# Kernel tuning notes

Measured on AMD Instinct MI355X. Metric: run time of the kernel, lower is better.

Reference implementation:

```python
import jax, jax.numpy as jnp
import numpy as np

N_NODES = 50000
N_EDGES = 800000
D_IN = 128
D_OUT = 128


def setup_inputs() -> dict:
    key = jax.random.key(0)
    k1, k2, k3, k4, k5 = jax.random.split(key, 5)
    # xavier-uniform-like scale for the two linear layers (gain for relu ~ sqrt(2))
    bound = float(np.sqrt(2.0) * np.sqrt(6.0 / (D_IN + D_OUT)))
    return {
        "feat": jax.random.normal(k1, (N_NODES, D_IN), dtype=jnp.float32),
        "w_neigh": jax.random.uniform(k2, (D_OUT, D_IN), minval=-bound, maxval=bound, dtype=jnp.float32),
        "w_self": jax.random.uniform(k3, (D_OUT, D_IN), minval=-bound, maxval=bound, dtype=jnp.float32),
        "b_self": jnp.zeros((D_OUT,), dtype=jnp.float32),
        "rows": jax.random.randint(k4, (N_EDGES,), 0, N_NODES, dtype=jnp.int32),  # src node per edge
        "cols": jax.random.randint(k5, (N_EDGES,), 0, N_NODES, dtype=jnp.int32),  # dst node per edge
    }


def reference(feat, w_neigh, w_self, b_self, rows, cols):
    n = feat.shape[0]
    # srcdata = fc_neigh(feat): [N, D_OUT]
    srcdata = feat @ w_neigh.T
    # deg[j] = A.sum(0)[j] = in-degree of destination j (column sums)
    deg = jax.ops.segment_sum(jnp.ones_like(cols, dtype=feat.dtype), cols, num_segments=n)
    # dstdata = (A @ diag(deg)^-1).T @ srcdata  ==  mean over incoming src neighbors
    agg = jax.ops.segment_sum(srcdata[rows], cols, num_segments=n)  # [N, D_OUT]
    dstdata = agg / jnp.where(deg > 0, deg, 1.0)[:, None]
    # rst = fc_self(h_self) + dstdata
    return feat @ w_self.T + b_self + dstdata
```

## Files before the change

kernel.cpp:

```cpp
#include <hip/hip_runtime.h>
#include <hip/hip_bf16.h>

#define D 128
#define CAP 64
#define TILE 64

typedef __attribute__((ext_vector_type(8))) short bf16x8;
typedef __attribute__((ext_vector_type(4))) float floatx4;

__device__ __forceinline__ unsigned short f2bf(float f) {
    unsigned int u = __float_as_uint(f);
    return (unsigned short)((u + 0x7fffu + ((u >> 16) & 1u)) >> 16);
}

__global__ __launch_bounds__(256) void zero_kernel(int* __restrict__ p, int n) {
    int i = blockIdx.x * 256 + threadIdx.x;
    if (i < n) p[i] = 0;
}

__global__ __launch_bounds__(256) void prep_fill_kernel(
    const float* __restrict__ feat,
    const float* __restrict__ w_self,
    const float* __restrict__ w_neigh,
    const int* __restrict__ rows,
    const int* __restrict__ cols,
    unsigned short* __restrict__ feat_h,
    unsigned short* __restrict__ ws_h,
    unsigned short* __restrict__ wn_h,
    int* __restrict__ cursor,
    unsigned short* __restrict__ slots,
    int n_nodes, int n_edges)
{
    const int b = blockIdx.x;
    const int tid = threadIdx.x;
    const int role = b % 3;

    if (role < 2) {
        int pb = (b / 3) * 2 + role;
        int i  = pb * 256 + tid;
        if (i < n_nodes * 32) {
            float4 v = *(const float4*)&feat[(long long)4 * i];
            ushort4 o;
            o.x = f2bf(v.x); o.y = f2bf(v.y); o.z = f2bf(v.z); o.w = f2bf(v.w);
            *(ushort4*)&feat_h[(long long)4 * i] = o;
        }
    } else {
        int fb = b / 3;
        int e  = fb * 256 + tid;
        if (e < n_edges) {
            int c = cols[e];
            int p = atomicAdd(&cursor[c], 1);
            if (p < CAP) slots[c * CAP + p] = (unsigned short)rows[e];
        }
        if (fb < 32) {
            int i = fb * 256 + tid;
            int j = i & 4095;
            const float* src = (i < 4096) ? w_self : w_neigh;
            unsigned short* dst = (i < 4096) ? ws_h : wn_h;
            float4 v = *(const float4*)&src[4 * j];
            ushort4 o;
            o.x = f2bf(v.x); o.y = f2bf(v.y); o.z = f2bf(v.z); o.w = f2bf(v.w);
            *(ushort4*)&dst[4 * j] = o;
        }
    }
}

__global__ __launch_bounds__(256, 4) void agg_gemm_kernel(
    const unsigned short* __restrict__ feat_h,
    const int* __restrict__ cursor,
    const unsigned short* __restrict__ slots,
    const unsigned short* __restrict__ ws_h,
    const unsigned short* __restrict__ wn_h,
    const float* __restrict__ b_self,
    float* __restrict__ out,
    int n_nodes)
{
    __shared__ unsigned short s_agg[TILE][136];

    const int tid  = threadIdx.x;
    const int row0 = blockIdx.x * TILE;

    {
        const int ln   = tid & 3;
        const int nl   = tid >> 2;
        const int node = row0 + nl;

        float acc[32];
        #pragma unroll
        for (int i = 0; i < 32; ++i) acc[i] = 0.f;

        int deg = 0;
        if (node < n_nodes) {
            deg = cursor[node];
            if (deg > CAP) deg = CAP;
            const unsigned short* slot = slots + (long long)node * CAP;
            for (int k = 0; k < deg; ++k) {
                int r = slot[k];
                const unsigned short* base = feat_h + (long long)r * D + ln * 32;
                uint4 v0 = *(const uint4*)(base + 0);
                uint4 v1 = *(const uint4*)(base + 8);
                uint4 v2 = *(const uint4*)(base + 16);
                uint4 v3 = *(const uint4*)(base + 24);
                const uint4 vv[4] = {v0, v1, v2, v3};
                #pragma unroll
                for (int c = 0; c < 4; ++c) {
                    acc[c * 8 + 0] += __uint_as_float(vv[c].x << 16);
                    acc[c * 8 + 1] += __uint_as_float(vv[c].x & 0xffff0000u);
                    acc[c * 8 + 2] += __uint_as_float(vv[c].y << 16);
                    acc[c * 8 + 3] += __uint_as_float(vv[c].y & 0xffff0000u);
                    acc[c * 8 + 4] += __uint_as_float(vv[c].z << 16);
                    acc[c * 8 + 5] += __uint_as_float(vv[c].z & 0xffff0000u);
                    acc[c * 8 + 6] += __uint_as_float(vv[c].w << 16);
                    acc[c * 8 + 7] += __uint_as_float(vv[c].w & 0xffff0000u);
                }
            }
            float inv = (deg > 0) ? 1.0f / (float)deg : 0.0f;
            #pragma unroll
            for (int c = 0; c < 4; ++c) {
                ushort4 o0, o1;
                o0.x = f2bf(acc[c * 8 + 0] * inv); o0.y = f2bf(acc[c * 8 + 1] * inv);
                o0.z = f2bf(acc[c * 8 + 2] * inv); o0.w = f2bf(acc[c * 8 + 3] * inv);
                o1.x = f2bf(acc[c * 8 + 4] * inv); o1.y = f2bf(acc[c * 8 + 5] * inv);
                o1.z = f2bf(acc[c * 8 + 6] * inv); o1.w = f2bf(acc[c * 8 + 7] * inv);
                *(ushort4*)&s_agg[nl][ln * 32 + c * 8]     = o0;
                *(ushort4*)&s_agg[nl][ln * 32 + c * 8 + 4] = o1;
            }
        } else {
            #pragma unroll
            for (int c = 0; c < 4; ++c) {
                *(ushort4*)&s_agg[nl][ln * 32 + c * 8]     = (ushort4){0,0,0,0};
                *(ushort4*)&s_agg[nl][ln * 32 + c * 8 + 4] = (ushort4){0,0,0,0};
            }
        }
    }
    __syncthreads();

    const int wave  = tid >> 6;
    const int lane  = tid & 63;
    const int m     = lane & 15;
    const int quad  = lane >> 4;
    const int kq    = quad * 8;
    const int rbase = row0 + wave * 16;

    floatx4 gacc[8];
    #pragma unroll
    for (int nt = 0; nt < 8; ++nt) gacc[nt] = (floatx4){0.f, 0.f, 0.f, 0.f};

    int rA = rbase + m;
    if (rA > n_nodes - 1) rA = n_nodes - 1;

    #pragma unroll
    for (int kt = 0; kt < 4; ++kt) {
        const int k = kt * 32 + kq;
        bf16x8 a = *(const bf16x8*)&feat_h[(long long)rA * D + k];
        #pragma unroll
        for (int nt = 0; nt < 8; ++nt) {
            bf16x8 b = *(const bf16x8*)&ws_h[(nt * 16 + m) * D + k];
            gacc[nt] = __builtin_amdgcn_mfma_f32_16x16x32_bf16(a, b, gacc[nt], 0, 0, 0);
        }
    }
    #pragma unroll
    for (int kt = 0; kt < 4; ++kt) {
        const int k = kt * 32 + kq;
        bf16x8 a = *(const bf16x8*)&s_agg[wave * 16 + m][k];
        #pragma unroll
        for (int nt = 0; nt < 8; ++nt) {
            bf16x8 b = *(const bf16x8*)&wn_h[(nt * 16 + m) * D + k];
            gacc[nt] = __builtin_amdgcn_mfma_f32_16x16x32_bf16(a, b, gacc[nt], 0, 0, 0);
        }
    }

    #pragma unroll
    for (int nt = 0; nt < 8; ++nt) {
        int col = nt * 16 + m;
        float bias = b_self[col];
        #pragma unroll
        for (int r = 0; r < 4; ++r) {
            int row = rbase + quad * 4 + r;
            if (row < n_nodes)
                out[(long long)row * D + col] = gacc[nt][r] + bias;
        }
    }
}

extern "C" void kernel_launch(void* const* d_in, const int* in_sizes, int n_in,
                              void* d_out, int out_size, void* d_ws, size_t ws_size,
                              hipStream_t stream) {
    const float* feat    = (const float*)d_in[0];
    const float* w_neigh = (const float*)d_in[1];
    const float* w_self  = (const float*)d_in[2];
    const float* b_self  = (const float*)d_in[3];
    const int*   rows    = (const int*)d_in[4];
    const int*   cols    = (const int*)d_in[5];
    float* out = (float*)d_out;

    const int n_nodes = in_sizes[0] / D;
    const int n_edges = in_sizes[4];

    unsigned short* feat_h = (unsigned short*)d_ws;
    unsigned short* slots  = feat_h + (size_t)n_nodes * D;
    int* cursor = (int*)(slots + (size_t)n_nodes * CAP);
    unsigned short* ws_h = (unsigned short*)(cursor + n_nodes);
    unsigned short* wn_h = ws_h + 16384;

    zero_kernel<<<(n_nodes + 255) / 256, 256, 0, stream>>>(cursor, n_nodes);

    int nblocks = (n_nodes * 32 + 255) / 256 + (n_edges + 255) / 256;
    prep_fill_kernel<<<nblocks, 256, 0, stream>>>(
        feat, w_self, w_neigh, rows, cols,
        feat_h, ws_h, wn_h, cursor, slots, n_nodes, n_edges);

    agg_gemm_kernel<<<(n_nodes + TILE - 1) / TILE, 256, 0, stream>>>(
        feat_h, cursor, slots, ws_h, wn_h, b_self, out, n_nodes);
}
```

Baseline: 193.4 us.

## Batch neighbor gathers with 8 lanes per node and halve row tile

The aggregation phase now gives each node 8 threads instead of 4, each owning 16 feature columns. Each thread loads 8 neighbor indices at once as a vector and issues up to 8 independent row gathers before accumulating, so more memory requests are in flight. The row tile drops from 64 to 32 nodes, giving more blocks, and the MFMA epilogue splits the 128 output columns across wave pairs. The cost is more blocks each doing less GEMM work and larger per-thread register buffers for the batched loads.

Measured after the change: 192.7 us. Within noise of the previous version (-0.4%).

```diff
diff --git a/kernel.cpp b/kernel.cpp
--- a/kernel.cpp
+++ b/kernel.cpp
@@ -3,7 +3,7 @@
 
 #define D 128
 #define CAP 64
-#define TILE 64
+#define TILE 32
 
 typedef __attribute__((ext_vector_type(8))) short bf16x8;
 typedef __attribute__((ext_vector_type(4))) float floatx4;
@@ -12,6 +12,8 @@
     unsigned int u = __float_as_uint(f);
     return (unsigned short)((u + 0x7fffu + ((u >> 16) & 1u)) >> 16);
 }
+__device__ __forceinline__ float bf_lo(unsigned int u) { return __uint_as_float(u << 16); }
+__device__ __forceinline__ float bf_hi(unsigned int u) { return __uint_as_float(u & 0xffff0000u); }
 
 __global__ __launch_bounds__(256) void zero_kernel(int* __restrict__ p, int n) {
     int i = blockIdx.x * 256 + threadIdx.x;
@@ -81,56 +83,66 @@
     const int row0 = blockIdx.x * TILE;
 
     {
-        const int ln   = tid & 3;
-        const int nl   = tid >> 2;
+        const int ln   = tid & 7;
+        const int nl   = tid >> 3;
         const int node = row0 + nl;
 
-        float acc[32];
-        #pragma unroll
-        for (int i = 0; i < 32; ++i) acc[i] = 0.f;
-
-        int deg = 0;
+        float acc[16];
+        #pragma unroll
+        for (int i = 0; i < 16; ++i) acc[i] = 0.f;
+
         if (node < n_nodes) {
-            deg = cursor[node];
+            int deg = cursor[node];
             if (deg > CAP) deg = CAP;
-            const unsigned short* slot = slots + (long long)node * CAP;
-            for (int k = 0; k < deg; ++k) {
-                int r = slot[k];
-                const unsigned short* base = feat_h + (long long)r * D + ln * 32;
-                uint4 v0 = *(const uint4*)(base + 0);
-                uint4 v1 = *(const uint4*)(base + 8);
-                uint4 v2 = *(const uint4*)(base + 16);
-                uint4 v3 = *(const uint4*)(base + 24);
-                const uint4 vv[4] = {v0, v1, v2, v3};
+            const unsigned short* slotp = slots + (long long)node * CAP;
+
+            for (int k0 = 0; k0 < deg; k0 += 8) {
+                uint4 sc = *(const uint4*)(slotp + k0);
+                unsigned int sv[4] = {sc.x, sc.y, sc.z, sc.w};
+                int cnt = deg - k0; if (cnt > 8) cnt = 8;
+
+                uint4 g[8][2];
                 #pragma unroll
-                for (int c = 0; c < 4; ++c) {
-                    acc[c * 8 + 0] += __uint_as_float(vv[c].x << 16);
-                    acc[c * 8 + 1] += __uint_as_float(vv[c].x & 0xffff0000u);
-                    acc[c * 8 + 2] += __uint_as_float(vv[c].y << 16);
-                    acc[c * 8 + 3] += __uint_as_float(vv[c].y & 0xffff0000u);
-                    acc[c * 8 + 4] += __uint_as_float(vv[c].z << 16);
-                    acc[c * 8 + 5] += __uint_as_float(vv[c].z & 0xffff0000u);
-                    acc[c * 8 + 6] += __uint_as_float(vv[c].w << 16);
-                    acc[c * 8 + 7] += __uint_as_float(vv[c].w & 0xffff0000u);
+                for (int j = 0; j < 8; ++j) {
+                    if (j < cnt) {
+                        int r = (int)((sv[j >> 1] >> ((j & 1) * 16)) & 0xffffu);
+                        const unsigned short* base = feat_h + (long long)r * D + ln * 16;
+                        g[j][0] = *(const uint4*)(base);
+                        g[j][1] = *(const uint4*)(base + 8);
+                    }
+                }
+                #pragma unroll
+                for (int j = 0; j < 8; ++j) {
+                    if (j < cnt) {
+                        #pragma unroll
+                        for (int c = 0; c < 2; ++c) {
+                            uint4 v = g[j][c];
+                            acc[c * 8 + 0] += bf_lo(v.x);
+                            acc[c * 8 + 1] += bf_hi(v.x);
+                            acc[c * 8 + 2] += bf_lo(v.y);
+                            acc[c * 8 + 3] += bf_hi(v.y);
+                            acc[c * 8 + 4] += bf_lo(v.z);
+                            acc[c * 8 + 5] += bf_hi(v.z);
+                            acc[c * 8 + 6] += bf_lo(v.w);
+                            acc[c * 8 + 7] += bf_hi(v.w);
+                        }
+                    }
                 }
             }
             float inv = (deg > 0) ? 1.0f / (float)deg : 0.0f;
             #pragma unroll
             for (int c = 0; c < 4; ++c) {
-                ushort4 o0, o1;
-                o0.x = f2bf(acc[c * 8 + 0] * inv); o0.y = f2bf(acc[c * 8 + 1] * inv);
-                o0.z = f2bf(acc[c * 8 + 2] * inv); o0.w = f2bf(acc[c * 8 + 3] * inv);
-                o1.x = f2bf(acc[c * 8 + 4] * inv); o1.y = f2bf(acc[c * 8 + 5] * inv);
-                o1.z = f2bf(acc[c * 8 + 6] * inv); o1.w = f2bf(acc[c * 8 + 7] * inv);
-                *(ushort4*)&s_agg[nl][ln * 32 + c * 8]     = o0;
-                *(ushort4*)&s_agg[nl][ln * 32 + c * 8 + 4] = o1;
+                ushort4 o;
+                o.x = f2bf(acc[c * 4 + 0] * inv);
+                o.y = f2bf(acc[c * 4 + 1] * inv);
+                o.z = f2bf(acc[c * 4 + 2] * inv);
+                o.w = f2bf(acc[c * 4 + 3] * inv);
+                *(ushort4*)&s_agg[nl][ln * 16 + c * 4] = o;
             }
         } else {
             #pragma unroll
-            for (int c = 0; c < 4; ++c) {
-                *(ushort4*)&s_agg[nl][ln * 32 + c * 8]     = (ushort4){0,0,0,0};
-                *(ushort4*)&s_agg[nl][ln * 32 + c * 8 + 4] = (ushort4){0,0,0,0};
-            }
+            for (int c = 0; c < 4; ++c)
+                *(ushort4*)&s_agg[nl][ln * 16 + c * 4] = (ushort4){0, 0, 0, 0};
         }
     }
     __syncthreads();
@@ -140,11 +152,13 @@
     const int m     = lane & 15;
     const int quad  = lane >> 4;
     const int kq    = quad * 8;
-    const int rbase = row0 + wave * 16;
-
-    floatx4 gacc[8];
-    #pragma unroll
-    for (int nt = 0; nt < 8; ++nt) gacc[nt] = (floatx4){0.f, 0.f, 0.f, 0.f};
+    const int rsub  = (wave & 1) * 16;
+    const int rbase = row0 + rsub;
+    const int cbase = (wave >> 1) * 64;
+
+    floatx4 gacc[4];
+    #pragma unroll
+    for (int nt = 0; nt < 4; ++nt) gacc[nt] = (floatx4){0.f, 0.f, 0.f, 0.f};
 
     int rA = rbase + m;
     if (rA > n_nodes - 1) rA = n_nodes - 1;
@@ -154,25 +168,25 @@
         const int k = kt * 32 + kq;
         bf16x8 a = *(const bf16x8*)&feat_h[(long long)rA * D + k];
         #pragma unroll
-        for (int nt = 0; nt < 8; ++nt) {
-            bf16x8 b = *(const bf16x8*)&ws_h[(nt * 16 + m) * D + k];
+        for (int nt = 0; nt < 4; ++nt) {
+            bf16x8 b = *(const bf16x8*)&ws_h[(cbase + nt * 16 + m) * D + k];
             gacc[nt] = __builtin_amdgcn_mfma_f32_16x16x32_bf16(a, b, gacc[nt], 0, 0, 0);
         }
     }
     #pragma unroll
     for (int kt = 0; kt < 4; ++kt) {
         const int k = kt * 32 + kq;
-        bf16x8 a = *(const bf16x8*)&s_agg[wave * 16 + m][k];
-        #pragma unroll
-        for (int nt = 0; nt < 8; ++nt) {
-            bf16x8 b = *(const bf16x8*)&wn_h[(nt * 16 + m) * D + k];
+        bf16x8 a = *(const bf16x8*)&s_agg[rsub + m][k];
+        #pragma unroll
+        for (int nt = 0; nt < 4; ++nt) {
+            bf16x8 b = *(const bf16x8*)&wn_h[(cbase + nt * 16 + m) * D + k];
             gacc[nt] = __builtin_amdgcn_mfma_f32_16x16x32_bf16(a, b, gacc[nt], 0, 0, 0);
         }
     }
 
     #pragma unroll
-    for (int nt = 0; nt < 8; ++nt) {
-        int col = nt * 16 + m;
+    for (int nt = 0; nt < 4; ++nt) {
+        int col = cbase + nt * 16 + m;
         float bias = b_self[col];
         #pragma unroll
         for (int r = 0; r < 4; ++r) {
```
